# Kernel optimization log

Hardware: AMD Instinct MI355X
Metric: run time of the kernel (lower is better)

Reference implementation:

```python
import jax, jax.numpy as jnp
import numpy as np
import math

B, L, D, ALPHA = 8, 4096, 1024, 64
EPS = 1e-6

def _xavier(key, shape):
    fan_in, fan_out = shape[1], shape[0]
    bound = math.sqrt(6.0 / (fan_in + fan_out))
    return jax.random.uniform(key, shape, jnp.float32, -bound, bound)

def layer_norm(x, g, b):
    # matches the torch module: unbiased std, divide by (std + eps)
    mean = jnp.mean(x, axis=-1, keepdims=True)
    var = jnp.sum((x - mean) ** 2, axis=-1, keepdims=True) / (x.shape[-1] - 1)
    std = jnp.sqrt(var)
    return g * (x - mean) / (std + EPS) + b

def setup_inputs() -> dict:
    key = jax.random.key(0)
    ks = jax.random.split(key, 8)
    x = jax.random.normal(ks[0], (B, L, D), jnp.float32)
    mask = jnp.ones((B, L), jnp.int32)
    W_Q = _xavier(ks[1], (D, D))          # torch Linear weight [out, in]
    b_Q = jnp.zeros((D,), jnp.float32)
    C_K = _xavier(ks[2], (D, ALPHA))
    C_V = _xavier(ks[3], (D, ALPHA))
    g1 = jnp.ones((D,), jnp.float32)
    be1 = jnp.zeros((D,), jnp.float32)
    Wc = _xavier(ks[4], (D, D))           # 1x1 conv weight squeezed: [out, in]
    bc = jax.random.normal(ks[5], (D,), jnp.float32) * 0.02
    g2 = jnp.ones((D,), jnp.float32)
    be2 = jnp.zeros((D,), jnp.float32)
    return {"x": x, "mask": mask, "W_Q": W_Q, "b_Q": b_Q, "C_K": C_K,
            "C_V": C_V, "g1": g1, "be1": be1, "Wc": Wc, "bc": bc,
            "g2": g2, "be2": be2}

def reference(x, mask, W_Q, b_Q, C_K, C_V, g1, be1, Wc, bc, g2, be2):
    d = x.shape[-1]
    # CoLAttention: Q = Linear(x); A = softmax(Q @ C_K / sqrt(D)); out = A @ C_V^T
    Q = jnp.einsum('bld,ed->ble', x, W_Q) + b_Q
    A = jax.nn.softmax(jnp.einsum('bld,da->bla', Q, C_K) / math.sqrt(d), axis=-1)
    A = A * mask[:, :, None].astype(A.dtype)
    attn = jnp.einsum('bla,da->bld', A, C_V)   # (dropout = 0)
    # Add & Norm
    h = layer_norm(x + attn, g1, be1)
    # PointWise 1x1 conv FFN: conv -> LeakyReLU -> (dropout=0) -> Add & Norm
    conv = jnp.einsum('bld,ed->ble', h, Wc) + bc
    act = jax.nn.leaky_relu(conv, negative_slope=0.01)
    out = layer_norm(h + act, g2, be2)
    return out
```

## Files before the change

### kernel.cpp

```cpp
#include <hip/hip_runtime.h>
#include <stdint.h>


#define NT 1024

typedef float  f32x4  __attribute__((ext_vector_type(4)));
typedef short  s16x8  __attribute__((ext_vector_type(8)));
typedef short  s16x4  __attribute__((ext_vector_type(4)));
typedef __bf16 bf16x8 __attribute__((ext_vector_type(8)));

__device__ __forceinline__ uint16_t f2bf(float f) {
  uint32_t b = __builtin_bit_cast(uint32_t, f);
  b += 0x7FFFu + ((b >> 16) & 1u);
  return (uint16_t)(b >> 16);
}
__device__ __forceinline__ float bf2f(uint16_t u) {
  return __builtin_bit_cast(float, ((uint32_t)u) << 16);
}
__device__ __forceinline__ f32x4 MFMA(s16x8 a, s16x8 b, f32x4 c) {
  return __builtin_amdgcn_mfma_f32_16x16x32_bf16(
      __builtin_bit_cast(bf16x8, a), __builtin_bit_cast(bf16x8, b), c, 0, 0, 0);
}

__global__ void k0_all(const float* __restrict__ WQ, const float* __restrict__ bQ,
                       const float* __restrict__ CK, const float* __restrict__ CV,
                       const float* __restrict__ Wc, const float* __restrict__ g1,
                       const float* __restrict__ be1, const float* __restrict__ bc,
                       uint16_t* __restrict__ MbfT, float* __restrict__ s0,
                       uint16_t* __restrict__ CVbf, uint16_t* __restrict__ Wpbf,
                       float* __restrict__ u, float* __restrict__ vb) {
  __shared__ float sm[2560];
  const int b = blockIdx.x, t = threadIdx.x;
  if (b < 64) {
    float (*wq)[16] = (float(*)[16])sm;
    float (*ck)[64] = (float(*)[64])(sm + 512);
    const int d0 = b * 16, a = t >> 2, dq = t & 3;
    float acc[4] = {0.f, 0.f, 0.f, 0.f};
    for (int e0 = 0; e0 < 1024; e0 += 32) {
      {
        int i0 = t * 2, r = i0 >> 4, c = i0 & 15;
        float2 v = *(const float2*)(WQ + (size_t)(e0 + r) * 1024 + d0 + c);
        wq[r][c] = v.x; wq[r][c + 1] = v.y;
      }
#pragma unroll
      for (int j = 0; j < 8; j++) {
        int idx = t + j * 256, r = idx >> 6, c = idx & 63;
        ck[r][c] = CK[(size_t)(e0 + r) * 64 + c];
      }
      __syncthreads();
      for (int r = 0; r < 32; r++) {
        float cv = ck[r][a];
#pragma unroll
        for (int i = 0; i < 4; i++) acc[i] += cv * wq[r][dq * 4 + i];
      }
      __syncthreads();
    }
#pragma unroll
    for (int i = 0; i < 4; i++)
      MbfT[(size_t)a * 1024 + d0 + dq * 4 + i] = f2bf(acc[i] * 0.03125f);
  } else if (b < 1152) {
    int i4 = (b - 64) * 256 + t;
    if (i4 < 16384) {
      float4 v = ((const float4*)CV)[i4];
      uint2 pk;
      pk.x = (uint32_t)f2bf(v.x) | ((uint32_t)f2bf(v.y) << 16);
      pk.y = (uint32_t)f2bf(v.z) | ((uint32_t)f2bf(v.w) << 16);
      *(uint2*)(CVbf + (size_t)i4 * 4) = pk;
    } else {
      int f4 = i4 - 16384;
      int d = (f4 * 4) & 1023;
      float4 v = ((const float4*)Wc)[f4];
      float4 g = *(const float4*)(g1 + d);
      v.x *= g.x; v.y *= g.y; v.z *= g.z; v.w *= g.w;
      uint2 pk;
      pk.x = (uint32_t)f2bf(v.x) | ((uint32_t)f2bf(v.y) << 16);
      pk.y = (uint32_t)f2bf(v.z) | ((uint32_t)f2bf(v.w) << 16);
      *(uint2*)(Wpbf + (size_t)f4 * 4) = pk;
    }
  } else if (b == 1152) {
    float (*part)[64] = (float(*)[64])sm;
    const int a = t & 63, q = t >> 6;
    float s = 0.f;
    for (int e = q * 256; e < (q + 1) * 256; e++) s += bQ[e] * CK[(size_t)e * 64 + a];
    part[q][a] = s;
    __syncthreads();
    if (q == 0) s0[a] = (part[0][a] + part[1][a] + part[2][a] + part[3][a]) * 0.03125f;
  } else {
    const int e = (b - 1153) * 4 + (t >> 6), l = t & 63;
    float su = 0.f, sv = 0.f;
#pragma unroll
    for (int j = 0; j < 16; j++) {
      int d = l + 64 * j;
      float w = Wc[(size_t)e * 1024 + d];
      su += g1[d] * w;
      sv += be1[d] * w;
    }
#pragma unroll
    for (int m = 1; m <= 32; m <<= 1) { su += __shfl_xor(su, m); sv += __shfl_xor(sv, m); }
    if (l == 0) { u[e] = su; vb[e] = sv + bc[e]; }
  }
}

__global__ __launch_bounds__(NT, 4) void fused_main(
    const float* __restrict__ x, const int* __restrict__ mask,
    const float* __restrict__ s0, const uint16_t* __restrict__ MbfT,
    const uint16_t* __restrict__ CVbf, const uint16_t* __restrict__ Wpbf,
    const float* __restrict__ u, const float* __restrict__ vb,
    const float* __restrict__ g1, const float* __restrict__ be1,
    const float* __restrict__ g2, const float* __restrict__ be2,
    float* __restrict__ out) {
  extern __shared__ char smem[];
  char*   xs    = smem;
  char*   asmb  = smem + 131072;
  float2* part  = (float2*)(smem + 139264);
  float*  stats = (float*)(smem + 147456);

  const int tid = threadIdx.x;
  const int w = tid >> 6, l = tid & 63;
  const int ln = l & 15, kg = l >> 4;
  const size_t tok0 = (size_t)blockIdx.x * 64;
  const int E0 = w * 64;

  {
    const float* xg = x + tok0 * 1024;
#pragma unroll
    for (int i = 0; i < 8; i++) {
      int g = tid + i * NT;
      int row = g >> 7, c8 = g & 127;
      const float4* p = (const float4*)(xg + (size_t)row * 1024 + c8 * 8);
      float vbuf[8];
      *(float4*)(vbuf) = p[0]; *(float4*)(vbuf + 4) = p[1];
      s16x8 pk;
#pragma unroll
      for (int e = 0; e < 8; e++) pk[e] = (short)f2bf(vbuf[e]);
      uint32_t ad = (uint32_t)(row * 2048 + c8 * 16) ^ ((uint32_t)(row & 7) << 4);
      *(s16x8*)(xs + ad) = pk;
    }
  }
  __syncthreads();

  if (w < 4) {
    const int tokr = w * 16 + ln;
    f32x4 accs[4];
#pragma unroll
    for (int at = 0; at < 4; at++) accs[at] = f32x4{0.f, 0.f, 0.f, 0.f};
    for (int ks = 0; ks < 32; ks++) {
      uint32_t ad = (uint32_t)(tokr * 2048 + ks * 64 + kg * 16) ^ ((uint32_t)(tokr & 7) << 4);
      s16x8 bfr = *(const s16x8*)(xs + ad);
#pragma unroll
      for (int at = 0; at < 4; at++) {
        s16x8 af = *(const s16x8*)(MbfT + (size_t)(at * 16 + ln) * 1024 + ks * 32 + kg * 8);
        accs[at] = MFMA(af, bfr, accs[at]);
      }
    }
    float v[4][4], mx = -1e30f;
#pragma unroll
    for (int at = 0; at < 4; at++) {
      float4 s4 = *(const float4*)(s0 + at * 16 + kg * 4);
      const float* sp = (const float*)&s4;
#pragma unroll
      for (int r = 0; r < 4; r++) { v[at][r] = accs[at][r] + sp[r]; mx = fmaxf(mx, v[at][r]); }
    }
    mx = fmaxf(mx, __shfl_xor(mx, 16));
    mx = fmaxf(mx, __shfl_xor(mx, 32));
    float s = 0.f;
#pragma unroll
    for (int at = 0; at < 4; at++)
#pragma unroll
      for (int r = 0; r < 4; r++) { v[at][r] = __expf(v[at][r] - mx); s += v[at][r]; }
    s += __shfl_xor(s, 16);
    s += __shfl_xor(s, 32);
    float inv = (float)mask[tok0 + tokr] / s;
#pragma unroll
    for (int at = 0; at < 4; at++) {
      s16x4 pk;
#pragma unroll
      for (int r = 0; r < 4; r++) pk[r] = (short)f2bf(v[at][r] * inv);
      uint32_t ad = (uint32_t)(tokr * 128 + at * 32 + kg * 8) ^ ((uint32_t)(tokr & 7) << 4);
      *(s16x4*)(asmb + ad) = pk;
    }
  }
  __syncthreads();

  float st[4], sq[4];
  {
    f32x4 acc[4][4];
#pragma unroll
    for (int et = 0; et < 4; et++)
#pragma unroll
      for (int tt = 0; tt < 4; tt++) acc[et][tt] = f32x4{0.f, 0.f, 0.f, 0.f};
#pragma unroll
    for (int ks = 0; ks < 2; ks++) {
      s16x8 bfr[4];
#pragma unroll
      for (int tt = 0; tt < 4; tt++) {
        int tokr = tt * 16 + ln;
        uint32_t ad = (uint32_t)(tokr * 128 + ks * 64 + kg * 16) ^ ((uint32_t)(tokr & 7) << 4);
        bfr[tt] = *(const s16x8*)(asmb + ad);
      }
#pragma unroll
      for (int et = 0; et < 4; et++) {
        s16x8 af = *(const s16x8*)(CVbf + (size_t)(E0 + et * 16 + ln) * 64 + ks * 32 + kg * 8);
#pragma unroll
        for (int tt = 0; tt < 4; tt++) acc[et][tt] = MFMA(af, bfr[tt], acc[et][tt]);
      }
    }
#pragma unroll
    for (int tt = 0; tt < 4; tt++) { st[tt] = 0.f; sq[tt] = 0.f; }
#pragma unroll
    for (int et = 0; et < 4; et++)
#pragma unroll
      for (int tt = 0; tt < 4; tt++) {
        int tokr = tt * 16 + ln;
        int d = E0 + et * 16 + kg * 4;
        uint32_t ad = (uint32_t)(tokr * 2048 + d * 2) ^ ((uint32_t)(tokr & 7) << 4);
        s16x4 xv = *(const s16x4*)(xs + ad);
        s16x4 hv;
#pragma unroll
        for (int r = 0; r < 4; r++) {
          float h = bf2f((uint16_t)xv[r]) + acc[et][tt][r];
          st[tt] += h; sq[tt] += h * h;
          hv[r] = (short)f2bf(h);
        }
        *(s16x4*)(xs + ad) = hv;
      }
#pragma unroll
    for (int tt = 0; tt < 4; tt++) {
      st[tt] += __shfl_xor(st[tt], 16); st[tt] += __shfl_xor(st[tt], 32);
      sq[tt] += __shfl_xor(sq[tt], 16); sq[tt] += __shfl_xor(sq[tt], 32);
    }
    if (kg == 0) {
#pragma unroll
      for (int tt = 0; tt < 4; tt++) part[w * 64 + tt * 16 + ln] = float2{st[tt], sq[tt]};
    }
  }
  __syncthreads();
  if (tid < 64) {
    float s = 0.f, q = 0.f;
#pragma unroll
    for (int ww = 0; ww < 16; ww++) { float2 p = part[ww * 64 + tid]; s += p.x; q += p.y; }
    float mean = s * (1.0f / 1024.0f);
    float var  = fmaxf((q - 1024.0f * mean * mean) * (1.0f / 1023.0f), 0.f);
    stats[tid * 2] = mean;
    stats[tid * 2 + 1] = 1.0f / (sqrtf(var) + 1e-6f);
  }
  __syncthreads();

  {
    f32x4 acc[4][4];
#pragma unroll
    for (int et = 0; et < 4; et++)
#pragma unroll
      for (int tt = 0; tt < 4; tt++) acc[et][tt] = f32x4{0.f, 0.f, 0.f, 0.f};
    for (int ks = 0; ks < 32; ks++) {
      s16x8 bfr[4];
#pragma unroll
      for (int tt = 0; tt < 4; tt++) {
        int tokr = tt * 16 + ln;
        uint32_t ad = (uint32_t)(tokr * 2048 + ks * 64 + kg * 16) ^ ((uint32_t)(tokr & 7) << 4);
        bfr[tt] = *(const s16x8*)(xs + ad);
      }
#pragma unroll
      for (int et = 0; et < 4; et++) {
        s16x8 af = *(const s16x8*)(Wpbf + (size_t)(E0 + et * 16 + ln) * 1024 + ks * 32 + kg * 8);
#pragma unroll
        for (int tt = 0; tt < 4; tt++) acc[et][tt] = MFMA(af, bfr[tt], acc[et][tt]);
      }
    }
#pragma unroll
    for (int tt = 0; tt < 4; tt++) { st[tt] = 0.f; sq[tt] = 0.f; }
#pragma unroll
    for (int et = 0; et < 4; et++) {
      int e0 = E0 + et * 16 + kg * 4;
      float4 u4 = *(const float4*)(u + e0);
      float4 v4 = *(const float4*)(vb + e0);
      float4 gg = *(const float4*)(g1 + e0);
      float4 bb = *(const float4*)(be1 + e0);
      const float *uf = (const float*)&u4, *vf = (const float*)&v4;
      const float *gf = (const float*)&gg, *bf = (const float*)&bb;
#pragma unroll
      for (int tt = 0; tt < 4; tt++) {
        int tokr = tt * 16 + ln;
        float mean = stats[tokr * 2], rinv = stats[tokr * 2 + 1];
        uint32_t ad = (uint32_t)(tokr * 2048 + e0 * 2) ^ ((uint32_t)(tokr & 7) << 4);
        s16x4 hv = *(const s16x4*)(xs + ad);
#pragma unroll
        for (int r = 0; r < 4; r++) {
          float conv = acc[et][tt][r] * rinv - rinv * mean * uf[r] + vf[r];
          float act  = conv > 0.f ? conv : 0.01f * conv;
          float h    = gf[r] * (bf2f((uint16_t)hv[r]) - mean) * rinv + bf[r];
          float rr   = h + act;
          acc[et][tt][r] = rr;
          st[tt] += rr; sq[tt] += rr * rr;
        }
      }
    }
#pragma unroll
    for (int tt = 0; tt < 4; tt++) {
      st[tt] += __shfl_xor(st[tt], 16); st[tt] += __shfl_xor(st[tt], 32);
      sq[tt] += __shfl_xor(sq[tt], 16); sq[tt] += __shfl_xor(sq[tt], 32);
    }
    if (kg == 0) {
#pragma unroll
      for (int tt = 0; tt < 4; tt++) part[w * 64 + tt * 16 + ln] = float2{st[tt], sq[tt]};
    }
    __syncthreads();
    if (tid < 64) {
      float s = 0.f, q = 0.f;
#pragma unroll
      for (int ww = 0; ww < 16; ww++) { float2 p = part[ww * 64 + tid]; s += p.x; q += p.y; }
      float mean = s * (1.0f / 1024.0f);
      float var  = fmaxf((q - 1024.0f * mean * mean) * (1.0f / 1023.0f), 0.f);
      stats[tid * 2] = mean;
      stats[tid * 2 + 1] = 1.0f / (sqrtf(var) + 1e-6f);
    }
    __syncthreads();

#pragma unroll
    for (int et = 0; et < 4; et++) {
      int e0 = E0 + et * 16 + kg * 4;
      float4 gg = *(const float4*)(g2 + e0);
      float4 bb = *(const float4*)(be2 + e0);
      const float *gf = (const float*)&gg, *bf = (const float*)&bb;
#pragma unroll
      for (int tt = 0; tt < 4; tt++) {
        int tokr = tt * 16 + ln;
        float mean = stats[tokr * 2], rinv = stats[tokr * 2 + 1];
        float4 o;
        o.x = gf[0] * (acc[et][tt][0] - mean) * rinv + bf[0];
        o.y = gf[1] * (acc[et][tt][1] - mean) * rinv + bf[1];
        o.z = gf[2] * (acc[et][tt][2] - mean) * rinv + bf[2];
        o.w = gf[3] * (acc[et][tt][3] - mean) * rinv + bf[3];
        *(float4*)(out + (tok0 + tokr) * 1024 + e0) = o;
      }
    }
  }
}

extern "C" void kernel_launch(void* const* d_in, const int* in_sizes, int n_in,
                              void* d_out, int out_size, void* d_ws, size_t ws_size,
                              hipStream_t stream) {
  const float* x   = (const float*)d_in[0];
  const int*   msk = (const int*)d_in[1];
  const float* WQ  = (const float*)d_in[2];
  const float* bQ  = (const float*)d_in[3];
  const float* CK  = (const float*)d_in[4];
  const float* CV  = (const float*)d_in[5];
  const float* g1  = (const float*)d_in[6];
  const float* be1 = (const float*)d_in[7];
  const float* Wc  = (const float*)d_in[8];
  const float* bc  = (const float*)d_in[9];
  const float* g2  = (const float*)d_in[10];
  const float* be2 = (const float*)d_in[11];
  float* out = (float*)d_out;

  char* ws = (char*)d_ws;
  uint16_t* Wpbf = (uint16_t*)ws;
  uint16_t* MbfT = (uint16_t*)(ws + 2097152);
  uint16_t* CVbf = (uint16_t*)(ws + 2228224);
  float*    s0   = (float*)(ws + 2359296);
  float*    u    = (float*)(ws + 2359552);
  float*    vb   = (float*)(ws + 2363648);

  (void)hipFuncSetAttribute((const void*)fused_main,
                            hipFuncAttributeMaxDynamicSharedMemorySize, 147968);

  k0_all<<<1409, 256, 0, stream>>>(WQ, bQ, CK, CV, Wc, g1, be1, bc,
                                   MbfT, s0, CVbf, Wpbf, u, vb);
  fused_main<<<512, NT, 147968, stream>>>(x, msk, s0, MbfT, CVbf, Wpbf,
                                          u, vb, g1, be1, g2, be2, out);
}
```

Measured before the change: 489.5 us.

## Halve token tile to 32 per block, 512 threads, redistribute softmax and output phases

Shrinks each block to 32 tokens and 8 waves, with each wave covering 128 output columns. This halves shared memory so two blocks can fit per CU, and doubles the grid to 1024 blocks. The softmax logits now go through shared memory so all waves share the score GEMM and the normalization. The pre-norm residual is stored back to LDS as bf16, and the final LayerNorm writes coalesced rows. The trade-offs are that each block re-reads the Wc weights for fewer tokens and the residual loses some precision from bf16 rounding.

```diff
diff --git a/kernel.cpp b/kernel.cpp
--- a/kernel.cpp
+++ b/kernel.cpp
@@ -2,7 +2,7 @@
 #include <stdint.h>
 
 
-#define NT 1024
+#define NT 512
 
 typedef float  f32x4  __attribute__((ext_vector_type(4)));
 typedef short  s16x8  __attribute__((ext_vector_type(8)));
@@ -111,15 +111,16 @@
     float* __restrict__ out) {
   extern __shared__ char smem[];
   char*   xs    = smem;
-  char*   asmb  = smem + 131072;
-  float2* part  = (float2*)(smem + 139264);
-  float*  stats = (float*)(smem + 147456);
+  char*   asmb  = smem + 65536;
+  float*  Ssm   = (float*)(smem + 69632);
+  float2* part  = (float2*)(smem + 69632);
+  float*  stats = (float*)(smem + 71680);
 
   const int tid = threadIdx.x;
   const int w = tid >> 6, l = tid & 63;
   const int ln = l & 15, kg = l >> 4;
-  const size_t tok0 = (size_t)blockIdx.x * 64;
-  const int E0 = w * 64;
+  const size_t tok0 = (size_t)blockIdx.x * 32;
+  const int E0 = w * 128;
 
   {
     const float* xg = x + tok0 * 1024;
@@ -139,78 +140,77 @@
   }
   __syncthreads();
 
-  if (w < 4) {
-    const int tokr = w * 16 + ln;
-    f32x4 accs[4];
-#pragma unroll
-    for (int at = 0; at < 4; at++) accs[at] = f32x4{0.f, 0.f, 0.f, 0.f};
+  {
+    const int at = w & 3, tt = w >> 2;
+    const int tokr = tt * 16 + ln;
+    f32x4 accs = {0.f, 0.f, 0.f, 0.f};
     for (int ks = 0; ks < 32; ks++) {
       uint32_t ad = (uint32_t)(tokr * 2048 + ks * 64 + kg * 16) ^ ((uint32_t)(tokr & 7) << 4);
       s16x8 bfr = *(const s16x8*)(xs + ad);
-#pragma unroll
-      for (int at = 0; at < 4; at++) {
-        s16x8 af = *(const s16x8*)(MbfT + (size_t)(at * 16 + ln) * 1024 + ks * 32 + kg * 8);
-        accs[at] = MFMA(af, bfr, accs[at]);
-      }
-    }
-    float v[4][4], mx = -1e30f;
-#pragma unroll
-    for (int at = 0; at < 4; at++) {
-      float4 s4 = *(const float4*)(s0 + at * 16 + kg * 4);
-      const float* sp = (const float*)&s4;
-#pragma unroll
-      for (int r = 0; r < 4; r++) { v[at][r] = accs[at][r] + sp[r]; mx = fmaxf(mx, v[at][r]); }
-    }
-    mx = fmaxf(mx, __shfl_xor(mx, 16));
-    mx = fmaxf(mx, __shfl_xor(mx, 32));
+      s16x8 af = *(const s16x8*)(MbfT + (size_t)(at * 16 + ln) * 1024 + ks * 32 + kg * 8);
+      accs = MFMA(af, bfr, accs);
+    }
+    float4 s4 = *(const float4*)(s0 + at * 16 + kg * 4);
+    const float* sp = (const float*)&s4;
+#pragma unroll
+    for (int r = 0; r < 4; r++)
+      Ssm[(at * 16 + kg * 4 + r) * 33 + tokr] = accs[r] + sp[r];
+  }
+  __syncthreads();
+
+  if (tid < 256) {
+    int token = tid >> 3, g8 = tid & 7;
+    float v[8];
+#pragma unroll
+    for (int i = 0; i < 8; i++) v[i] = Ssm[(g8 * 8 + i) * 33 + token];
+    float m = v[0];
+#pragma unroll
+    for (int i = 1; i < 8; i++) m = fmaxf(m, v[i]);
+    m = fmaxf(m, __shfl_xor(m, 1));
+    m = fmaxf(m, __shfl_xor(m, 2));
+    m = fmaxf(m, __shfl_xor(m, 4));
     float s = 0.f;
 #pragma unroll
-    for (int at = 0; at < 4; at++)
-#pragma unroll
-      for (int r = 0; r < 4; r++) { v[at][r] = __expf(v[at][r] - mx); s += v[at][r]; }
-    s += __shfl_xor(s, 16);
-    s += __shfl_xor(s, 32);
-    float inv = (float)mask[tok0 + tokr] / s;
-#pragma unroll
-    for (int at = 0; at < 4; at++) {
-      s16x4 pk;
-#pragma unroll
-      for (int r = 0; r < 4; r++) pk[r] = (short)f2bf(v[at][r] * inv);
-      uint32_t ad = (uint32_t)(tokr * 128 + at * 32 + kg * 8) ^ ((uint32_t)(tokr & 7) << 4);
-      *(s16x4*)(asmb + ad) = pk;
-    }
-  }
-  __syncthreads();
-
-  float st[4], sq[4];
-  {
-    f32x4 acc[4][4];
-#pragma unroll
-    for (int et = 0; et < 4; et++)
-#pragma unroll
-      for (int tt = 0; tt < 4; tt++) acc[et][tt] = f32x4{0.f, 0.f, 0.f, 0.f};
+    for (int i = 0; i < 8; i++) { v[i] = __expf(v[i] - m); s += v[i]; }
+    s += __shfl_xor(s, 1); s += __shfl_xor(s, 2); s += __shfl_xor(s, 4);
+    float inv = (float)mask[tok0 + token] / s;
+    s16x8 pk;
+#pragma unroll
+    for (int i = 0; i < 8; i++) pk[i] = (short)f2bf(v[i] * inv);
+    uint32_t ad = (uint32_t)(token * 128 + g8 * 16) ^ ((uint32_t)(token & 7) << 4);
+    *(s16x8*)(asmb + ad) = pk;
+  }
+  __syncthreads();
+
+  float st[2], sq[2];
+  {
+    f32x4 acc[8][2];
+#pragma unroll
+    for (int et = 0; et < 8; et++)
+#pragma unroll
+      for (int tt = 0; tt < 2; tt++) acc[et][tt] = f32x4{0.f, 0.f, 0.f, 0.f};
 #pragma unroll
     for (int ks = 0; ks < 2; ks++) {
-      s16x8 bfr[4];
-#pragma unroll
-      for (int tt = 0; tt < 4; tt++) {
+      s16x8 bfr[2];
+#pragma unroll
+      for (int tt = 0; tt < 2; tt++) {
         int tokr = tt * 16 + ln;
         uint32_t ad = (uint32_t)(tokr * 128 + ks * 64 + kg * 16) ^ ((uint32_t)(tokr & 7) << 4);
         bfr[tt] = *(const s16x8*)(asmb + ad);
       }
 #pragma unroll
-      for (int et = 0; et < 4; et++) {
+      for (int et = 0; et < 8; et++) {
         s16x8 af = *(const s16x8*)(CVbf + (size_t)(E0 + et * 16 + ln) * 64 + ks * 32 + kg * 8);
 #pragma unroll
-        for (int tt = 0; tt < 4; tt++) acc[et][tt] = MFMA(af, bfr[tt], acc[et][tt]);
-      }
-    }
-#pragma unroll
-    for (int tt = 0; tt < 4; tt++) { st[tt] = 0.f; sq[tt] = 0.f; }
-#pragma unroll
-    for (int et = 0; et < 4; et++)
-#pragma unroll
-      for (int tt = 0; tt < 4; tt++) {
+        for (int tt = 0; tt < 2; tt++) acc[et][tt] = MFMA(af, bfr[tt], acc[et][tt]);
+      }
+    }
+#pragma unroll
+    for (int tt = 0; tt < 2; tt++) { st[tt] = 0.f; sq[tt] = 0.f; }
+#pragma unroll
+    for (int et = 0; et < 8; et++)
+#pragma unroll
+      for (int tt = 0; tt < 2; tt++) {
         int tokr = tt * 16 + ln;
         int d = E0 + et * 16 + kg * 4;
         uint32_t ad = (uint32_t)(tokr * 2048 + d * 2) ^ ((uint32_t)(tokr & 7) << 4);
@@ -225,20 +225,20 @@
         *(s16x4*)(xs + ad) = hv;
       }
 #pragma unroll
-    for (int tt = 0; tt < 4; tt++) {
+    for (int tt = 0; tt < 2; tt++) {
       st[tt] += __shfl_xor(st[tt], 16); st[tt] += __shfl_xor(st[tt], 32);
       sq[tt] += __shfl_xor(sq[tt], 16); sq[tt] += __shfl_xor(sq[tt], 32);
     }
     if (kg == 0) {
 #pragma unroll
-      for (int tt = 0; tt < 4; tt++) part[w * 64 + tt * 16 + ln] = float2{st[tt], sq[tt]};
-    }
-  }
-  __syncthreads();
-  if (tid < 64) {
+      for (int tt = 0; tt < 2; tt++) part[w * 32 + tt * 16 + ln] = float2{st[tt], sq[tt]};
+    }
+  }
+  __syncthreads();
+  if (tid < 32) {
     float s = 0.f, q = 0.f;
 #pragma unroll
-    for (int ww = 0; ww < 16; ww++) { float2 p = part[ww * 64 + tid]; s += p.x; q += p.y; }
+    for (int ww = 0; ww < 8; ww++) { float2 p = part[ww * 32 + tid]; s += p.x; q += p.y; }
     float mean = s * (1.0f / 1024.0f);
     float var  = fmaxf((q - 1024.0f * mean * mean) * (1.0f / 1023.0f), 0.f);
     stats[tid * 2] = mean;
@@ -247,30 +247,31 @@
   __syncthreads();
 
   {
-    f32x4 acc[4][4];
-#pragma unroll
-    for (int et = 0; et < 4; et++)
-#pragma unroll
-      for (int tt = 0; tt < 4; tt++) acc[et][tt] = f32x4{0.f, 0.f, 0.f, 0.f};
+    f32x4 acc[8][2];
+#pragma unroll
+    for (int et = 0; et < 8; et++)
+#pragma unroll
+      for (int tt = 0; tt < 2; tt++) acc[et][tt] = f32x4{0.f, 0.f, 0.f, 0.f};
     for (int ks = 0; ks < 32; ks++) {
-      s16x8 bfr[4];
-#pragma unroll
-      for (int tt = 0; tt < 4; tt++) {
+      s16x8 bfr[2];
+#pragma unroll
+      for (int tt = 0; tt < 2; tt++) {
         int tokr = tt * 16 + ln;
         uint32_t ad = (uint32_t)(tokr * 2048 + ks * 64 + kg * 16) ^ ((uint32_t)(tokr & 7) << 4);
         bfr[tt] = *(const s16x8*)(xs + ad);
       }
 #pragma unroll
-      for (int et = 0; et < 4; et++) {
+      for (int et = 0; et < 8; et++) {
         s16x8 af = *(const s16x8*)(Wpbf + (size_t)(E0 + et * 16 + ln) * 1024 + ks * 32 + kg * 8);
 #pragma unroll
-        for (int tt = 0; tt < 4; tt++) acc[et][tt] = MFMA(af, bfr[tt], acc[et][tt]);
-      }
-    }
-#pragma unroll
-    for (int tt = 0; tt < 4; tt++) { st[tt] = 0.f; sq[tt] = 0.f; }
-#pragma unroll
-    for (int et = 0; et < 4; et++) {
+        for (int tt = 0; tt < 2; tt++) acc[et][tt] = MFMA(af, bfr[tt], acc[et][tt]);
+      }
+    }
+    __syncthreads();
+#pragma unroll
+    for (int tt = 0; tt < 2; tt++) { st[tt] = 0.f; sq[tt] = 0.f; }
+#pragma unroll
+    for (int et = 0; et < 8; et++) {
       int e0 = E0 + et * 16 + kg * 4;
       float4 u4 = *(const float4*)(u + e0);
       float4 v4 = *(const float4*)(vb + e0);
@@ -279,60 +280,62 @@
       const float *uf = (const float*)&u4, *vf = (const float*)&v4;
       const float *gf = (const float*)&gg, *bf = (const float*)&bb;
 #pragma unroll
-      for (int tt = 0; tt < 4; tt++) {
+      for (int tt = 0; tt < 2; tt++) {
         int tokr = tt * 16 + ln;
         float mean = stats[tokr * 2], rinv = stats[tokr * 2 + 1];
         uint32_t ad = (uint32_t)(tokr * 2048 + e0 * 2) ^ ((uint32_t)(tokr & 7) << 4);
         s16x4 hv = *(const s16x4*)(xs + ad);
+        s16x4 rv;
 #pragma unroll
         for (int r = 0; r < 4; r++) {
           float conv = acc[et][tt][r] * rinv - rinv * mean * uf[r] + vf[r];
           float act  = conv > 0.f ? conv : 0.01f * conv;
           float h    = gf[r] * (bf2f((uint16_t)hv[r]) - mean) * rinv + bf[r];
           float rr   = h + act;
-          acc[et][tt][r] = rr;
+          rv[r] = (short)f2bf(rr);
           st[tt] += rr; sq[tt] += rr * rr;
         }
-      }
-    }
-#pragma unroll
-    for (int tt = 0; tt < 4; tt++) {
+        *(s16x4*)(xs + ad) = rv;
+      }
+    }
+#pragma unroll
+    for (int tt = 0; tt < 2; tt++) {
       st[tt] += __shfl_xor(st[tt], 16); st[tt] += __shfl_xor(st[tt], 32);
       sq[tt] += __shfl_xor(sq[tt], 16); sq[tt] += __shfl_xor(sq[tt], 32);
     }
     if (kg == 0) {
 #pragma unroll
-      for (int tt = 0; tt < 4; tt++) part[w * 64 + tt * 16 + ln] = float2{st[tt], sq[tt]};
-    }
-    __syncthreads();
-    if (tid < 64) {
-      float s = 0.f, q = 0.f;
-#pragma unroll
-      for (int ww = 0; ww < 16; ww++) { float2 p = part[ww * 64 + tid]; s += p.x; q += p.y; }
-      float mean = s * (1.0f / 1024.0f);
-      float var  = fmaxf((q - 1024.0f * mean * mean) * (1.0f / 1023.0f), 0.f);
-      stats[tid * 2] = mean;
-      stats[tid * 2 + 1] = 1.0f / (sqrtf(var) + 1e-6f);
-    }
-    __syncthreads();
-
-#pragma unroll
-    for (int et = 0; et < 4; et++) {
-      int e0 = E0 + et * 16 + kg * 4;
-      float4 gg = *(const float4*)(g2 + e0);
-      float4 bb = *(const float4*)(be2 + e0);
-      const float *gf = (const float*)&gg, *bf = (const float*)&bb;
-#pragma unroll
-      for (int tt = 0; tt < 4; tt++) {
-        int tokr = tt * 16 + ln;
-        float mean = stats[tokr * 2], rinv = stats[tokr * 2 + 1];
-        float4 o;
-        o.x = gf[0] * (acc[et][tt][0] - mean) * rinv + bf[0];
-        o.y = gf[1] * (acc[et][tt][1] - mean) * rinv + bf[1];
-        o.z = gf[2] * (acc[et][tt][2] - mean) * rinv + bf[2];
-        o.w = gf[3] * (acc[et][tt][3] - mean) * rinv + bf[3];
-        *(float4*)(out + (tok0 + tokr) * 1024 + e0) = o;
-      }
+      for (int tt = 0; tt < 2; tt++) part[w * 32 + tt * 16 + ln] = float2{st[tt], sq[tt]};
+    }
+  }
+  __syncthreads();
+  if (tid < 32) {
+    float s = 0.f, q = 0.f;
+#pragma unroll
+    for (int ww = 0; ww < 8; ww++) { float2 p = part[ww * 32 + tid]; s += p.x; q += p.y; }
+    float mean = s * (1.0f / 1024.0f);
+    float var  = fmaxf((q - 1024.0f * mean * mean) * (1.0f / 1023.0f), 0.f);
+    stats[tid * 2] = mean;
+    stats[tid * 2 + 1] = 1.0f / (sqrtf(var) + 1e-6f);
+  }
+  __syncthreads();
+
+  {
+#pragma unroll
+    for (int i = 0; i < 16; i++) {
+      int g = tid + i * NT;
+      int row = g >> 8, c4 = g & 255;
+      uint32_t ad = (uint32_t)(row * 2048 + c4 * 8) ^ ((uint32_t)(row & 7) << 4);
+      s16x4 vv = *(const s16x4*)(xs + ad);
+      float mean = stats[row * 2], rinv = stats[row * 2 + 1];
+      float4 gg = *(const float4*)(g2 + c4 * 4);
+      float4 bb = *(const float4*)(be2 + c4 * 4);
+      float4 o;
+      o.x = gg.x * (bf2f((uint16_t)vv[0]) - mean) * rinv + bb.x;
+      o.y = gg.y * (bf2f((uint16_t)vv[1]) - mean) * rinv + bb.y;
+      o.z = gg.z * (bf2f((uint16_t)vv[2]) - mean) * rinv + bb.z;
+      o.w = gg.w * (bf2f((uint16_t)vv[3]) - mean) * rinv + bb.w;
+      *(float4*)(out + (tok0 + row) * 1024 + c4 * 4) = o;
     }
   }
 }
@@ -363,10 +366,10 @@
   float*    vb   = (float*)(ws + 2363648);
 
   (void)hipFuncSetAttribute((const void*)fused_main,
-                            hipFuncAttributeMaxDynamicSharedMemorySize, 147968);
+                            hipFuncAttributeMaxDynamicSharedMemorySize, 78080);
 
   k0_all<<<1409, 256, 0, stream>>>(WQ, bQ, CK, CV, Wc, g1, be1, bc,
                                    MbfT, s0, CVbf, Wpbf, u, vb);
-  fused_main<<<512, NT, 147968, stream>>>(x, msk, s0, MbfT, CVbf, Wpbf,
+  fused_main<<<1024, NT, 78080, stream>>>(x, msk, s0, MbfT, CVbf, Wpbf,
                                           u, vb, g1, be1, g2, be2, out);
 }
```

Result: slower. 561.2 us (+14.7%).
